# Kernel tuning notes

Measured on AMD Instinct MI355X. Metric: run time of the kernel, lower is better.

The kernel has to match this reference:

```python
import jax, jax.numpy as jnp
import numpy as np

N, E, F_IN, H, EF, G, GFD = 50000, 800000, 64, 128, 8, 10, 2
NEG_SLOPE = 0.2  # PyG GATv2Conv default negative_slope


def _gatv2_layer(x, src, dst, edge_attr, Wl, bl, Wr, br, We, att, bias):
    # PyG GATv2Conv, heads=1, concat=True, share_weights=False
    n = x.shape[0]
    xl = x @ Wl + bl            # source transform [N,H]
    xr = x @ Wr + br            # target transform [N,H]
    e = edge_attr @ We          # edge embedding   [E,H]
    s = jax.nn.leaky_relu(xl[src] + xr[dst] + e, NEG_SLOPE)  # [E,H]
    logits = s @ att            # [E]
    # numerically-stable segment softmax over destination nodes
    mx = jax.ops.segment_max(logits, dst, num_segments=n)
    mx = jnp.where(jnp.isfinite(mx), mx, 0.0)
    ex = jnp.exp(logits - mx[dst])
    den = jax.ops.segment_sum(ex, dst, num_segments=n)
    alpha = ex / jnp.maximum(den[dst], 1e-16)
    out = jax.ops.segment_sum(alpha[:, None] * xl[src], dst, num_segments=n)
    return out + bias


def _forward(x, edge_index, edge_attr, graph_features, num_graphs, params, head_W, head_b):
    src, dst = edge_index[0], edge_index[1]
    for (Wl, bl, Wr, br, We, att, bias) in params:
        x = jax.nn.relu(_gatv2_layer(x, src, dst, edge_attr, Wl, bl, Wr, br, We, att, bias))
        # dropout p=0.0 / eval mode: no-op
    n_nodes = x.shape[0] // num_graphs
    # faithful replication of the torch reshape chain (graph_feature_dim == 2):
    # graph_features.T [GFD,G] -> unsqueeze(2) -> repeat to [GFD,G,Np] -> view(G,GFD,Np)
    # -> cat(unbind(0), dim=1) -> [GFD, G*Np]
    gf = jnp.broadcast_to(graph_features.T[:, :, None], (GFD, num_graphs, n_nodes))
    gf = gf.reshape(num_graphs, GFD, n_nodes)
    gf = gf.transpose(1, 0, 2).reshape(GFD, num_graphs * n_nodes)
    x = jnp.concatenate([x, gf.T], axis=1)  # [N, H+GFD]
    return x @ head_W + head_b


def setup_inputs():
    key = jax.random.key(0)
    ks = list(jax.random.split(key, 32))
    p = lambda k, s: jax.random.normal(k, s, jnp.float32) * 0.05
    inp = {
        'x': jax.random.normal(ks[0], (N, F_IN), jnp.float32),
        'edge_index': jax.random.randint(ks[1], (2, E), 0, N),
        'edge_attr': jax.random.normal(ks[2], (E, EF), jnp.float32),
        'graph_features': jax.random.normal(ks[3], (G, GFD), jnp.float32),
        'num_graphs': G,
    }
    i = 4
    for l in range(3):
        fin = F_IN if l == 0 else H
        inp[f'Wl{l}'] = p(ks[i], (fin, H)); i += 1
        inp[f'bl{l}'] = jnp.zeros((H,), jnp.float32)
        inp[f'Wr{l}'] = p(ks[i], (fin, H)); i += 1
        inp[f'br{l}'] = jnp.zeros((H,), jnp.float32)
        inp[f'We{l}'] = p(ks[i], (EF, H)); i += 1
        inp[f'att{l}'] = p(ks[i], (H,)); i += 1
        inp[f'bias{l}'] = jnp.zeros((H,), jnp.float32)
    inp['head_W'] = p(ks[i], (H + GFD, 1))
    inp['head_b'] = jnp.zeros((1,), jnp.float32)
    return inp


def reference(x, edge_index, edge_attr, graph_features, num_graphs,
              Wl0, bl0, Wr0, br0, We0, att0, bias0,
              Wl1, bl1, Wr1, br1, We1, att1, bias1,
              Wl2, bl2, Wr2, br2, We2, att2, bias2,
              head_W, head_b):
    params = [(Wl0, bl0, Wr0, br0, We0, att0, bias0),
              (Wl1, bl1, Wr1, br1, We1, att1, bias1),
              (Wl2, bl2, Wr2, br2, We2, att2, bias2)]
    return _forward(x, edge_index, edge_attr, graph_features, num_graphs, params, head_W, head_b)
```

## Files before the change

### kernel.cpp

```cpp
#include <hip/hip_runtime.h>
#include <hip/hip_bf16.h>
#include <math.h>

#define NN 50000
#define EE 800000
#define F_IN 64
#define HH 128
#define EF 8
#define GG 10
#define GFD 2
#define NEG_SLOPE 0.2f
#define NB 64

__device__ __forceinline__ void fma4(float4& a, float s, const float4& b) {
  a.x = fmaf(s, b.x, a.x); a.y = fmaf(s, b.y, a.y);
  a.z = fmaf(s, b.z, a.z); a.w = fmaf(s, b.w, a.w);
}
__device__ __forceinline__ float lrelu1(float x) {
  return fmaxf(x, NEG_SLOPE * x);
}

template <int CTRL>
__device__ __forceinline__ float dpp_add(float v) {
  int p = __builtin_amdgcn_update_dpp(0, __float_as_int(v), CTRL, 0xf, 0xf, true);
  return v + __int_as_float(p);
}
__device__ __forceinline__ float red32(float v) {
  v = dpp_add<0xB1>(v);
  v = dpp_add<0x4E>(v);
  v = dpp_add<0x141>(v);
  v = dpp_add<0x140>(v);
  v += __int_as_float(__builtin_amdgcn_ds_swizzle(__float_as_int(v), 0x401F));
  return v;
}

__global__ __launch_bounds__(256) void lin2_kernel(
    const float* __restrict__ x, int fin,
    const float* __restrict__ Wl, const float* __restrict__ bl,
    const float* __restrict__ Wr, const float* __restrict__ br,
    float* __restrict__ xl, float* __restrict__ xr, int n_nodes) {
  __shared__ float xs[64 * 128];
  const int tid = threadIdx.x;
  const int base = blockIdx.x * 64;
  int nrows = n_nodes - base; if (nrows > 64) nrows = 64;

  const int total4 = (nrows * fin) >> 2;
  const float4* xsrc = (const float4*)(x + (size_t)base * fin);
  float4* xd = (float4*)xs;
  for (int i = tid; i < total4; i += 256) xd[i] = xsrc[i];
  __syncthreads();

  const int lane = tid & 63;
  const int w = tid >> 6;
  const int c = lane * 2;

  float accl0[16], accl1[16], accr0[16], accr1[16];
#pragma unroll
  for (int j = 0; j < 16; j++) { accl0[j]=0.f; accl1[j]=0.f; accr0[j]=0.f; accr1[j]=0.f; }

  const float* xrow = xs + (w * 16) * fin;
  for (int k = 0; k < fin; k += 4) {
    float2 wl0 = *(const float2*)(Wl + (size_t)k * HH + c);
    float2 wl1 = *(const float2*)(Wl + (size_t)(k + 1) * HH + c);
    float2 wl2 = *(const float2*)(Wl + (size_t)(k + 2) * HH + c);
    float2 wl3 = *(const float2*)(Wl + (size_t)(k + 3) * HH + c);
    float2 wr0 = *(const float2*)(Wr + (size_t)k * HH + c);
    float2 wr1 = *(const float2*)(Wr + (size_t)(k + 1) * HH + c);
    float2 wr2 = *(const float2*)(Wr + (size_t)(k + 2) * HH + c);
    float2 wr3 = *(const float2*)(Wr + (size_t)(k + 3) * HH + c);
#pragma unroll
    for (int j = 0; j < 16; j++) {
      float4 xv = *(const float4*)(xrow + j * fin + k);
      accl0[j] = fmaf(xv.x, wl0.x, accl0[j]);
      accl1[j] = fmaf(xv.x, wl0.y, accl1[j]);
      accr0[j] = fmaf(xv.x, wr0.x, accr0[j]);
      accr1[j] = fmaf(xv.x, wr0.y, accr1[j]);
      accl0[j] = fmaf(xv.y, wl1.x, accl0[j]);
      accl1[j] = fmaf(xv.y, wl1.y, accl1[j]);
      accr0[j] = fmaf(xv.y, wr1.x, accr0[j]);
      accr1[j] = fmaf(xv.y, wr1.y, accr1[j]);
      accl0[j] = fmaf(xv.z, wl2.x, accl0[j]);
      accl1[j] = fmaf(xv.z, wl2.y, accl1[j]);
      accr0[j] = fmaf(xv.z, wr2.x, accr0[j]);
      accr1[j] = fmaf(xv.z, wr2.y, accr1[j]);
      accl0[j] = fmaf(xv.w, wl3.x, accl0[j]);
      accl1[j] = fmaf(xv.w, wl3.y, accl1[j]);
      accr0[j] = fmaf(xv.w, wr3.x, accr0[j]);
      accr1[j] = fmaf(xv.w, wr3.y, accr1[j]);
    }
  }
  float2 blv = *(const float2*)(bl + c);
  float2 brv = *(const float2*)(br + c);
#pragma unroll
  for (int j = 0; j < 16; j++) {
    int n = base + w * 16 + j;
    if (n < n_nodes) {
      *(float2*)(xl + (size_t)n * HH + c) = make_float2(accl0[j] + blv.x, accl1[j] + blv.y);
      *(float2*)(xr + (size_t)n * HH + c) = make_float2(accr0[j] + brv.x, accr1[j] + brv.y);
    }
  }
}

__global__ __launch_bounds__(256) void hist_kernel(const int* __restrict__ dst,
                                                   int* __restrict__ hist, int ne) {
  int i = blockIdx.x * blockDim.x + threadIdx.x;
  if (i < ne) atomicAdd(&hist[dst[i]], 1);
}

__global__ __launch_bounds__(1024) void reduce_kernel(const int* __restrict__ hist,
                                                      int* __restrict__ bsum, int n) {
  __shared__ int wsum[16];
  const int tid = threadIdx.x;
  const int lane = tid & 63, w = tid >> 6;
  int i = blockIdx.x * 1024 + tid;
  int v = (i < n) ? hist[i] : 0;
#pragma unroll
  for (int off = 32; off; off >>= 1) v += __shfl_xor(v, off);
  if (lane == 0) wsum[w] = v;
  __syncthreads();
  if (tid < 16) {
    int s = wsum[tid];
#pragma unroll
    for (int off = 8; off; off >>= 1) s += __shfl_xor(s, off);
    if (tid == 0) bsum[blockIdx.x] = s;
  }
}

__global__ __launch_bounds__(64) void scanb_kernel(const int* __restrict__ bsum,
                                                   int* __restrict__ bbase,
                                                   int* __restrict__ offs, int nb, int n) {
  const int tid = threadIdx.x;
  int v = (tid < nb) ? bsum[tid] : 0;
  int inc = v;
#pragma unroll
  for (int d = 1; d < 64; d <<= 1) {
    int t2 = __shfl_up(inc, d);
    if (tid >= d) inc += t2;
  }
  if (tid < nb) bbase[tid] = inc - v;
  if (tid == 63) offs[n] = inc;
}

__global__ __launch_bounds__(1024) void scanc_kernel(const int* __restrict__ hist,
                                                     const int* __restrict__ bbase,
                                                     int* __restrict__ offs,
                                                     int* __restrict__ cursor, int n) {
  __shared__ int wsum[16], wpre[16];
  const int tid = threadIdx.x;
  const int lane = tid & 63, w = tid >> 6;
  int i = blockIdx.x * 1024 + tid;
  int orig = (i < n) ? hist[i] : 0;
  int v = orig;
#pragma unroll
  for (int d = 1; d < 64; d <<= 1) {
    int t2 = __shfl_up(v, d);
    if (lane >= d) v += t2;
  }
  if (lane == 63) wsum[w] = v;
  __syncthreads();
  if (tid < 16) {
    int s = wsum[tid];
    int inc = s;
#pragma unroll
    for (int d = 1; d < 16; d <<= 1) {
      int t2 = __shfl_up(inc, d);
      if (tid >= d) inc += t2;
    }
    wpre[tid] = inc - s;
  }
  __syncthreads();
  if (i < n) {
    int ex = bbase[blockIdx.x] + wpre[w] + (v - orig);
    offs[i] = ex; cursor[i] = ex;
  }
}

__global__ __launch_bounds__(256) void scatter_kernel(
    const int* __restrict__ src, const int* __restrict__ dst,
    int* __restrict__ cursor, int* __restrict__ pk,
    const float4* __restrict__ ea4, float4* __restrict__ eas, int ne) {
  int i = blockIdx.x * blockDim.x + threadIdx.x;
  if (i < ne) {
    int d = dst[i];
    int pos = atomicAdd(&cursor[d], 1);
    pk[pos] = src[i] * 512;
    float4 a = ea4[i * 2], b = ea4[i * 2 + 1];
    eas[pos * 2] = a; eas[pos * 2 + 1] = b;
  }
}

__global__ __launch_bounds__(256) void deg_hist_kernel(const int* __restrict__ offs,
                                                       int* __restrict__ hist2, int n) {
  __shared__ int lhist[NB];
  const int tid = threadIdx.x;
  int i = blockIdx.x * 256 + tid;
  if (tid < NB) lhist[tid] = 0;
  __syncthreads();
  if (i < n) {
    int d = offs[i + 1] - offs[i];
    int key = NB - 1 - min(d, NB - 1);
    atomicAdd(&lhist[key], 1);
  }
  __syncthreads();
  if (tid < NB && lhist[tid]) atomicAdd(&hist2[tid], lhist[tid]);
}

__global__ __launch_bounds__(64) void scan64_kernel(const int* __restrict__ hist2,
                                                    int* __restrict__ cursor2) {
  const int tid = threadIdx.x;
  int v = hist2[tid];
  int inc = v;
#pragma unroll
  for (int d = 1; d < 64; d <<= 1) {
    int t2 = __shfl_up(inc, d);
    if (tid >= d) inc += t2;
  }
  cursor2[tid] = inc - v;
}

__global__ __launch_bounds__(256) void deg_scatter_kernel(const int* __restrict__ offs,
                                                          int* __restrict__ cursor2,
                                                          int4* __restrict__ meta4, int n) {
  __shared__ int lhist[NB];
  __shared__ int lbase[NB];
  const int tid = threadIdx.x;
  int i = blockIdx.x * 256 + tid;
  if (tid < NB) lhist[tid] = 0;
  __syncthreads();
  int key = 0, rank = 0, bb = 0, ee = 0;
  const bool valid = (i < n);
  if (valid) {
    bb = offs[i]; ee = offs[i + 1];
    int d = ee - bb;
    key = NB - 1 - min(d, NB - 1);
    rank = atomicAdd(&lhist[key], 1);
  }
  __syncthreads();
  if (tid < NB && lhist[tid]) lbase[tid] = atomicAdd(&cursor2[tid], lhist[tid]);
  __syncthreads();
  if (valid) meta4[lbase[key] + rank] = make_int4(bb, ee, i, 0);
}

__global__ __launch_bounds__(256, 4) void gat_fused_kernel(
    const float* __restrict__ xl, const float* __restrict__ xr,
    const float* __restrict__ eas, const float* __restrict__ We,
    const float* __restrict__ att,
    const int* __restrict__ pk, const int4* __restrict__ meta4,
    const float* __restrict__ bias,
    float* __restrict__ xout, int n_nodes,
    float* __restrict__ out_head, const float* __restrict__ hw,
    const float* __restrict__ hb) {
  const int lane = threadIdx.x & 63;
  const int g = lane >> 5, t = lane & 31;
  const int c = t * 4;
  const int tb = t * 16;
  const int nwaves = gridDim.x * 4;

  float4 we[EF];
#pragma unroll
  for (int k = 0; k < EF; k++) we[k] = *(const float4*)(We + k * HH + c);
  const float4 at = *(const float4*)(att + c);
  const float4 bi = *(const float4*)(bias + c);
  const char* xlb = (const char*)xl;
  const char* easb = (const char*)eas;
  float4 hwv = make_float4(0.f, 0.f, 0.f, 0.f);
  float hw0 = 0.f, hw1 = 0.f, hb0 = 0.f;
  if (out_head) {
    hwv = *(const float4*)(hw + c);
    hw0 = hw[HH]; hw1 = hw[HH + 1]; hb0 = hb[0];
  }

  int wid = blockIdx.x * 4 + (threadIdx.x >> 6);
  if (wid >= n_nodes) return;
  int4 mt = meta4[wid];
  float4 vr = *(const float4*)(xr + (size_t)mt.z * HH + c);

  while (true) {
    const int b = mt.x, e = mt.y, node = mt.z;
    const int deg = e - b;
    const int nwid = wid + nwaves;
    const bool hasN = nwid < n_nodes;
    int4 mtN = mt;
    if (hasN) mtN = meta4[nwid];

    float4 o;
    if (deg == 0) {
      o.x = fmaxf(bi.x, 0.f); o.y = fmaxf(bi.y, 0.f);
      o.z = fmaxf(bi.z, 0.f); o.w = fmaxf(bi.w, 0.f);
    } else {
      const int emax = e - 1;
      float4 acc = make_float4(0.f, 0.f, 0.f, 0.f);
      float den = 0.f;
      float4 vlA, eaPA, eaQA, vlB, eaPB, eaQB;

#define LOADS(VL, EP, EQ, IDX)                                      \
  do {                                                              \
    int _cx = min((IDX), emax);                                     \
    EP = *(const float4*)(easb + (_cx << 5));                       \
    EQ = *(const float4*)(easb + (_cx << 5) + 16);                  \
    int _ob = pk[_cx];                                              \
    VL = *(const float4*)(xlb + (_ob + tb));                        \
  } while (0)

#define PROCESS(VL, EP, EQ, IDX)                                     \
  do {                                                               \
    float4 s = make_float4(VL.x + vr.x, VL.y + vr.y, VL.z + vr.z,    \
                           VL.w + vr.w);                             \
    fma4(s, EP.x, we[0]); fma4(s, EP.y, we[1]);                      \
    fma4(s, EP.z, we[2]); fma4(s, EP.w, we[3]);                      \
    fma4(s, EQ.x, we[4]); fma4(s, EQ.y, we[5]);                      \
    fma4(s, EQ.z, we[6]); fma4(s, EQ.w, we[7]);                      \
    float v = lrelu1(s.x) * at.x;                                    \
    v = fmaf(lrelu1(s.y), at.y, v);                                  \
    v = fmaf(lrelu1(s.z), at.z, v);                                  \
    v = fmaf(lrelu1(s.w), at.w, v);                                  \
    v = red32(v);                                                    \
    const float p = ((IDX) < e) ? __expf(v) : 0.f;                   \
    den += p;                                                        \
    fma4(acc, p, VL);                                                \
  } while (0)

      int idx = b + g;
      LOADS(vlA, eaPA, eaQA, idx);
      LOADS(vlB, eaPB, eaQB, idx + 2);

      const int nit = (deg + 3) >> 2;
      for (int j = 0; j < nit; j++) {
        PROCESS(vlA, eaPA, eaQA, idx);
        LOADS(vlA, eaPA, eaQA, idx + 4);
        PROCESS(vlB, eaPB, eaQB, idx + 2);
        LOADS(vlB, eaPB, eaQB, idx + 6);
        idx += 4;
      }
#undef LOADS
#undef PROCESS

      den += __shfl_xor(den, 32);
      acc.x += __shfl_xor(acc.x, 32);
      acc.y += __shfl_xor(acc.y, 32);
      acc.z += __shfl_xor(acc.z, 32);
      acc.w += __shfl_xor(acc.w, 32);

      const float inv = 1.f / fmaxf(den, 1e-16f);
      o.x = fmaxf(fmaf(acc.x, inv, bi.x), 0.f);
      o.y = fmaxf(fmaf(acc.y, inv, bi.y), 0.f);
      o.z = fmaxf(fmaf(acc.z, inv, bi.z), 0.f);
      o.w = fmaxf(fmaf(acc.w, inv, bi.w), 0.f);
    }

    float4 vrN = vr;
    if (hasN) vrN = *(const float4*)(xr + (size_t)mtN.z * HH + c);

    if (!out_head) {
      if (g == 0) *(float4*)(xout + (size_t)node * HH + c) = o;
    } else {
      float hv = o.x * hwv.x + o.y * hwv.y + o.z * hwv.z + o.w * hwv.w;
      hv = red32(hv);
      if (lane == 0) {
        int k = node / (NN / GG);
        int i0 = 2 * k, i1 = 2 * k + 1;
        float gf0 = xout[(i0 % GG) * GFD + (i0 / GG)];
        float gf1 = xout[(i1 % GG) * GFD + (i1 / GG)];
        out_head[node] = hv + gf0 * hw0 + gf1 * hw1 + hb0;
      }
    }

    if (!hasN) break;
    wid = nwid; mt = mtN; vr = vrN;
  }
}

extern "C" void kernel_launch(void* const* d_in, const int* in_sizes, int n_in,
                              void* d_out, int out_size, void* d_ws, size_t ws_size,
                              hipStream_t stream) {
  const float* x_in = (const float*)d_in[0];
  const int*   eidx = (const int*)d_in[1];
  const float* ea   = (const float*)d_in[2];
  const float* gf   = (const float*)d_in[3];
  const int* src = eidx;
  const int* dst = eidx + EE;
  const float* head_W = (const float*)d_in[26];
  const float* head_b = (const float*)d_in[27];
  float* out = (float*)d_out;

  const int NCHUNK = (NN + 1023) / 1024;

  float* P      = (float*)d_ws;
  float* Q      = P + (size_t)NN * HH;
  float* R      = Q + (size_t)NN * HH;
  float* eas    = R + (size_t)NN * HH;
  int*   pk     = (int*)(eas + (size_t)EE * EF);
  int*   hist   = pk + EE;
  int*   offs   = hist + NN;
  int*   cursor = offs + NN + 1;
  int*   hist2  = cursor + NN;
  int*   cursor2= hist2 + NB;
  int*   bsum   = cursor2 + NB;
  int*   bbase  = bsum + NCHUNK;
  int4*  meta4  = (int4*)(((size_t)(bbase + NCHUNK) + 15) & ~(size_t)15);

  (void)hipMemsetAsync(hist, 0, NN * sizeof(int), stream);
  (void)hipMemsetAsync(hist2, 0, NB * sizeof(int), stream);
  hist_kernel<<<(EE + 255) / 256, 256, 0, stream>>>(dst, hist, EE);
  reduce_kernel<<<NCHUNK, 1024, 0, stream>>>(hist, bsum, NN);
  scanb_kernel<<<1, 64, 0, stream>>>(bsum, bbase, offs, NCHUNK, NN);
  scanc_kernel<<<NCHUNK, 1024, 0, stream>>>(hist, bbase, offs, cursor, NN);
  scatter_kernel<<<(EE + 255) / 256, 256, 0, stream>>>(src, dst, cursor, pk,
                                                       (const float4*)ea, (float4*)eas, EE);
  deg_hist_kernel<<<(NN + 255) / 256, 256, 0, stream>>>(offs, hist2, NN);
  scan64_kernel<<<1, 64, 0, stream>>>(hist2, cursor2);
  deg_scatter_kernel<<<(NN + 255) / 256, 256, 0, stream>>>(offs, cursor2, meta4, NN);

  const float* xcur = x_in;
  int fin = F_IN;
  for (int l = 0; l < 3; l++) {
    const float* Wl   = (const float*)d_in[5 + 7 * l + 0];
    const float* bl   = (const float*)d_in[5 + 7 * l + 1];
    const float* Wr   = (const float*)d_in[5 + 7 * l + 2];
    const float* br   = (const float*)d_in[5 + 7 * l + 3];
    const float* We   = (const float*)d_in[5 + 7 * l + 4];
    const float* att  = (const float*)d_in[5 + 7 * l + 5];
    const float* bias = (const float*)d_in[5 + 7 * l + 6];

    lin2_kernel<<<(NN + 63) / 64, 256, 0, stream>>>(xcur, fin, Wl, bl, Wr, br, P, Q, NN);
    if (l < 2) {
      gat_fused_kernel<<<2048, 256, 0, stream>>>(P, Q, eas, We, att, pk, meta4,
                                                 bias, R, NN, nullptr, nullptr, nullptr);
    } else {
      gat_fused_kernel<<<2048, 256, 0, stream>>>(P, Q, eas, We, att, pk, meta4,
                                                 bias, (float*)gf, NN, out, head_W, head_b);
    }
    xcur = R;
    fin = HH;
  }
}
```

Before: 494.5 us.

## Fuse independent preprocessing kernels and use packed v2f math in GAT edge loop

Merges the layer-0 linear transform with the destination histogram into one launch, and the edge scatter with the degree histogram into another, selecting the role by block index. This cuts kernel launches and lets independent work share the GPU. The two histogram buffers become adjacent so a single memset clears both. The GAT edge loop is rewritten with 2-wide float vectors and elementwise FMA so the compiler can emit packed FP32 instructions, at the cost of more register shuffling and possible pressure under the 4-blocks launch bound.

```diff
diff --git a/kernel.cpp b/kernel.cpp
--- a/kernel.cpp
+++ b/kernel.cpp
@@ -12,10 +12,12 @@
 #define NEG_SLOPE 0.2f
 #define NB 64
 
-__device__ __forceinline__ void fma4(float4& a, float s, const float4& b) {
-  a.x = fmaf(s, b.x, a.x); a.y = fmaf(s, b.y, a.y);
-  a.z = fmaf(s, b.z, a.z); a.w = fmaf(s, b.w, a.w);
-}
+typedef float v2f __attribute__((ext_vector_type(2)));
+__device__ __forceinline__ v2f fma2(v2f a, v2f b, v2f c) {
+  return __builtin_elementwise_fma(a, b, c);
+}
+__device__ __forceinline__ v2f bc2(float x) { v2f r; r.x = x; r.y = x; return r; }
+
 __device__ __forceinline__ float lrelu1(float x) {
   return fmaxf(x, NEG_SLOPE * x);
 }
@@ -34,14 +36,14 @@
   return v;
 }
 
-__global__ __launch_bounds__(256) void lin2_kernel(
-    const float* __restrict__ x, int fin,
+__device__ __forceinline__ void lin2_body(
+    int bid, const float* __restrict__ x, int fin,
     const float* __restrict__ Wl, const float* __restrict__ bl,
     const float* __restrict__ Wr, const float* __restrict__ br,
     float* __restrict__ xl, float* __restrict__ xr, int n_nodes) {
   __shared__ float xs[64 * 128];
   const int tid = threadIdx.x;
-  const int base = blockIdx.x * 64;
+  const int base = bid * 64;
   int nrows = n_nodes - base; if (nrows > 64) nrows = 64;
 
   const int total4 = (nrows * fin) >> 2;
@@ -101,10 +103,30 @@
   }
 }
 
-__global__ __launch_bounds__(256) void hist_kernel(const int* __restrict__ dst,
-                                                   int* __restrict__ hist, int ne) {
-  int i = blockIdx.x * blockDim.x + threadIdx.x;
+__global__ __launch_bounds__(256) void lin2_kernel(
+    const float* __restrict__ x, int fin,
+    const float* __restrict__ Wl, const float* __restrict__ bl,
+    const float* __restrict__ Wr, const float* __restrict__ br,
+    float* __restrict__ xl, float* __restrict__ xr, int n_nodes) {
+  lin2_body(blockIdx.x, x, fin, Wl, bl, Wr, br, xl, xr, n_nodes);
+}
+
+__device__ __forceinline__ void hist_body(int bid, const int* __restrict__ dst,
+                                          int* __restrict__ hist, int ne) {
+  int i = bid * 256 + threadIdx.x;
   if (i < ne) atomicAdd(&hist[dst[i]], 1);
+}
+
+__global__ __launch_bounds__(256) void fusedA_kernel(
+    int nl2, const float* __restrict__ x, int fin,
+    const float* __restrict__ Wl, const float* __restrict__ bl,
+    const float* __restrict__ Wr, const float* __restrict__ br,
+    float* __restrict__ xl, float* __restrict__ xr, int n_nodes,
+    const int* __restrict__ dst, int* __restrict__ hist, int ne) {
+  if ((int)blockIdx.x < nl2)
+    lin2_body(blockIdx.x, x, fin, Wl, bl, Wr, br, xl, xr, n_nodes);
+  else
+    hist_body(blockIdx.x - nl2, dst, hist, ne);
 }
 
 __global__ __launch_bounds__(1024) void reduce_kernel(const int* __restrict__ hist,
@@ -175,11 +197,11 @@
   }
 }
 
-__global__ __launch_bounds__(256) void scatter_kernel(
-    const int* __restrict__ src, const int* __restrict__ dst,
+__device__ __forceinline__ void scatter_body(
+    int bid, const int* __restrict__ src, const int* __restrict__ dst,
     int* __restrict__ cursor, int* __restrict__ pk,
     const float4* __restrict__ ea4, float4* __restrict__ eas, int ne) {
-  int i = blockIdx.x * blockDim.x + threadIdx.x;
+  int i = bid * 256 + threadIdx.x;
   if (i < ne) {
     int d = dst[i];
     int pos = atomicAdd(&cursor[d], 1);
@@ -189,11 +211,11 @@
   }
 }
 
-__global__ __launch_bounds__(256) void deg_hist_kernel(const int* __restrict__ offs,
-                                                       int* __restrict__ hist2, int n) {
+__device__ __forceinline__ void deg_hist_body(int bid, const int* __restrict__ offs,
+                                              int* __restrict__ hist2, int n) {
   __shared__ int lhist[NB];
   const int tid = threadIdx.x;
-  int i = blockIdx.x * 256 + tid;
+  int i = bid * 256 + tid;
   if (tid < NB) lhist[tid] = 0;
   __syncthreads();
   if (i < n) {
@@ -203,6 +225,17 @@
   }
   __syncthreads();
   if (tid < NB && lhist[tid]) atomicAdd(&hist2[tid], lhist[tid]);
+}
+
+__global__ __launch_bounds__(256) void fusedB_kernel(
+    int nsc, const int* __restrict__ src, const int* __restrict__ dst,
+    int* __restrict__ cursor, int* __restrict__ pk,
+    const float4* __restrict__ ea4, float4* __restrict__ eas, int ne,
+    const int* __restrict__ offs, int* __restrict__ hist2, int n) {
+  if ((int)blockIdx.x < nsc)
+    scatter_body(blockIdx.x, src, dst, cursor, pk, ea4, eas, ne);
+  else
+    deg_hist_body(blockIdx.x - nsc, offs, hist2, n);
 }
 
 __global__ __launch_bounds__(64) void scan64_kernel(const int* __restrict__ hist2,
@@ -256,9 +289,13 @@
   const int tb = t * 16;
   const int nwaves = gridDim.x * 4;
 
-  float4 we[EF];
-#pragma unroll
-  for (int k = 0; k < EF; k++) we[k] = *(const float4*)(We + k * HH + c);
+  v2f wea[EF], web[EF];
+#pragma unroll
+  for (int k = 0; k < EF; k++) {
+    float4 w4 = *(const float4*)(We + k * HH + c);
+    wea[k].x = w4.x; wea[k].y = w4.y;
+    web[k].x = w4.z; web[k].y = w4.w;
+  }
   const float4 at = *(const float4*)(att + c);
   const float4 bi = *(const float4*)(bias + c);
   const char* xlb = (const char*)xl;
@@ -273,7 +310,7 @@
   int wid = blockIdx.x * 4 + (threadIdx.x >> 6);
   if (wid >= n_nodes) return;
   int4 mt = meta4[wid];
-  float4 vr = *(const float4*)(xr + (size_t)mt.z * HH + c);
+  float4 vr4 = *(const float4*)(xr + (size_t)mt.z * HH + c);
 
   while (true) {
     const int b = mt.x, e = mt.y, node = mt.z;
@@ -283,72 +320,88 @@
     int4 mtN = mt;
     if (hasN) mtN = meta4[nwid];
 
+    v2f vra; vra.x = vr4.x; vra.y = vr4.y;
+    v2f vrb; vrb.x = vr4.z; vrb.y = vr4.w;
+
     float4 o;
     if (deg == 0) {
       o.x = fmaxf(bi.x, 0.f); o.y = fmaxf(bi.y, 0.f);
       o.z = fmaxf(bi.z, 0.f); o.w = fmaxf(bi.w, 0.f);
     } else {
       const int emax = e - 1;
-      float4 acc = make_float4(0.f, 0.f, 0.f, 0.f);
+      v2f acc0 = bc2(0.f), acc1 = bc2(0.f);
       float den = 0.f;
-      float4 vlA, eaPA, eaQA, vlB, eaPB, eaQB;
-
-#define LOADS(VL, EP, EQ, IDX)                                      \
+      v2f vlAa, vlAb, epA0, epA1, eqA0, eqA1;
+      v2f vlBa, vlBb, epB0, epB1, eqB0, eqB1;
+
+#define LOADS(VLa, VLb, P0, P1, Q0, Q1, IDX)                        \
   do {                                                              \
     int _cx = min((IDX), emax);                                     \
-    EP = *(const float4*)(easb + (_cx << 5));                       \
-    EQ = *(const float4*)(easb + (_cx << 5) + 16);                  \
+    float4 _ep = *(const float4*)(easb + (_cx << 5));               \
+    float4 _eq = *(const float4*)(easb + (_cx << 5) + 16);          \
     int _ob = pk[_cx];                                              \
-    VL = *(const float4*)(xlb + (_ob + tb));                        \
+    float4 _vl = *(const float4*)(xlb + (_ob + tb));                \
+    P0.x = _ep.x; P0.y = _ep.y; P1.x = _ep.z; P1.y = _ep.w;         \
+    Q0.x = _eq.x; Q0.y = _eq.y; Q1.x = _eq.z; Q1.y = _eq.w;         \
+    VLa.x = _vl.x; VLa.y = _vl.y; VLb.x = _vl.z; VLb.y = _vl.w;     \
   } while (0)
 
-#define PROCESS(VL, EP, EQ, IDX)                                     \
+#define PROCESS(VLa, VLb, P0, P1, Q0, Q1, IDX)                       \
   do {                                                               \
-    float4 s = make_float4(VL.x + vr.x, VL.y + vr.y, VL.z + vr.z,    \
-                           VL.w + vr.w);                             \
-    fma4(s, EP.x, we[0]); fma4(s, EP.y, we[1]);                      \
-    fma4(s, EP.z, we[2]); fma4(s, EP.w, we[3]);                      \
-    fma4(s, EQ.x, we[4]); fma4(s, EQ.y, we[5]);                      \
-    fma4(s, EQ.z, we[6]); fma4(s, EQ.w, we[7]);                      \
-    float v = lrelu1(s.x) * at.x;                                    \
-    v = fmaf(lrelu1(s.y), at.y, v);                                  \
-    v = fmaf(lrelu1(s.z), at.z, v);                                  \
-    v = fmaf(lrelu1(s.w), at.w, v);                                  \
+    v2f s0 = VLa + vra;                                              \
+    v2f s1 = VLb + vrb;                                              \
+    s0 = fma2(bc2(P0.x), wea[0], s0); s1 = fma2(bc2(P0.x), web[0], s1); \
+    s0 = fma2(bc2(P0.y), wea[1], s0); s1 = fma2(bc2(P0.y), web[1], s1); \
+    s0 = fma2(bc2(P1.x), wea[2], s0); s1 = fma2(bc2(P1.x), web[2], s1); \
+    s0 = fma2(bc2(P1.y), wea[3], s0); s1 = fma2(bc2(P1.y), web[3], s1); \
+    s0 = fma2(bc2(Q0.x), wea[4], s0); s1 = fma2(bc2(Q0.x), web[4], s1); \
+    s0 = fma2(bc2(Q0.y), wea[5], s0); s1 = fma2(bc2(Q0.y), web[5], s1); \
+    s0 = fma2(bc2(Q1.x), wea[6], s0); s1 = fma2(bc2(Q1.x), web[6], s1); \
+    s0 = fma2(bc2(Q1.y), wea[7], s0); s1 = fma2(bc2(Q1.y), web[7], s1); \
+    v2f m0 = s0 * bc2(NEG_SLOPE);                                    \
+    v2f m1 = s1 * bc2(NEG_SLOPE);                                    \
+    float l0 = fmaxf(s0.x, m0.x), l1 = fmaxf(s0.y, m0.y);            \
+    float l2 = fmaxf(s1.x, m1.x), l3 = fmaxf(s1.y, m1.y);            \
+    float v = l0 * at.x;                                             \
+    v = fmaf(l1, at.y, v);                                           \
+    v = fmaf(l2, at.z, v);                                           \
+    v = fmaf(l3, at.w, v);                                           \
     v = red32(v);                                                    \
     const float p = ((IDX) < e) ? __expf(v) : 0.f;                   \
     den += p;                                                        \
-    fma4(acc, p, VL);                                                \
+    acc0 = fma2(bc2(p), VLa, acc0);                                  \
+    acc1 = fma2(bc2(p), VLb, acc1);                                  \
   } while (0)
 
       int idx = b + g;
-      LOADS(vlA, eaPA, eaQA, idx);
-      LOADS(vlB, eaPB, eaQB, idx + 2);
+      LOADS(vlAa, vlAb, epA0, epA1, eqA0, eqA1, idx);
+      LOADS(vlBa, vlBb, epB0, epB1, eqB0, eqB1, idx + 2);
 
       const int nit = (deg + 3) >> 2;
       for (int j = 0; j < nit; j++) {
-        PROCESS(vlA, eaPA, eaQA, idx);
-        LOADS(vlA, eaPA, eaQA, idx + 4);
-        PROCESS(vlB, eaPB, eaQB, idx + 2);
-        LOADS(vlB, eaPB, eaQB, idx + 6);
+        PROCESS(vlAa, vlAb, epA0, epA1, eqA0, eqA1, idx);
+        LOADS(vlAa, vlAb, epA0, epA1, eqA0, eqA1, idx + 4);
+        PROCESS(vlBa, vlBb, epB0, epB1, eqB0, eqB1, idx + 2);
+        LOADS(vlBa, vlBb, epB0, epB1, eqB0, eqB1, idx + 6);
         idx += 4;
       }
 #undef LOADS
 #undef PROCESS
 
       den += __shfl_xor(den, 32);
-      acc.x += __shfl_xor(acc.x, 32);
-      acc.y += __shfl_xor(acc.y, 32);
-      acc.z += __shfl_xor(acc.z, 32);
-      acc.w += __shfl_xor(acc.w, 32);
+      float a0 = acc0.x + __shfl_xor(acc0.x, 32);
+      float a1 = acc0.y + __shfl_xor(acc0.y, 32);
+      float a2 = acc1.x + __shfl_xor(acc1.x, 32);
+      float a3 = acc1.y + __shfl_xor(acc1.y, 32);
 
       const float inv = 1.f / fmaxf(den, 1e-16f);
-      o.x = fmaxf(fmaf(acc.x, inv, bi.x), 0.f);
-      o.y = fmaxf(fmaf(acc.y, inv, bi.y), 0.f);
-      o.z = fmaxf(fmaf(acc.z, inv, bi.z), 0.f);
-      o.w = fmaxf(fmaf(acc.w, inv, bi.w), 0.f);
-    }
-
-    float4 vrN = vr;
+      o.x = fmaxf(fmaf(a0, inv, bi.x), 0.f);
+      o.y = fmaxf(fmaf(a1, inv, bi.y), 0.f);
+      o.z = fmaxf(fmaf(a2, inv, bi.z), 0.f);
+      o.w = fmaxf(fmaf(a3, inv, bi.w), 0.f);
+    }
+
+    float4 vrN = vr4;
     if (hasN) vrN = *(const float4*)(xr + (size_t)mtN.z * HH + c);
 
     if (!out_head) {
@@ -366,7 +419,7 @@
     }
 
     if (!hasN) break;
-    wid = nwid; mt = mtN; vr = vrN;
+    wid = nwid; mt = mtN; vr4 = vrN;
   }
 }
 
@@ -384,6 +437,9 @@
   float* out = (float*)d_out;
 
   const int NCHUNK = (NN + 1023) / 1024;
+  const int NL2B = (NN + 63) / 64;
+  const int NHB  = (EE + 255) / 256;
+  const int NDB  = (NN + 255) / 256;
 
   float* P      = (float*)d_ws;
   float* Q      = P + (size_t)NN * HH;
@@ -391,38 +447,41 @@
   float* eas    = R + (size_t)NN * HH;
   int*   pk     = (int*)(eas + (size_t)EE * EF);
   int*   hist   = pk + EE;
-  int*   offs   = hist + NN;
+  int*   hist2  = hist + NN;
+  int*   offs   = hist2 + NB;
   int*   cursor = offs + NN + 1;
-  int*   hist2  = cursor + NN;
-  int*   cursor2= hist2 + NB;
+  int*   cursor2= cursor + NN;
   int*   bsum   = cursor2 + NB;
   int*   bbase  = bsum + NCHUNK;
   int4*  meta4  = (int4*)(((size_t)(bbase + NCHUNK) + 15) & ~(size_t)15);
 
-  (void)hipMemsetAsync(hist, 0, NN * sizeof(int), stream);
-  (void)hipMemsetAsync(hist2, 0, NB * sizeof(int), stream);
-  hist_kernel<<<(EE + 255) / 256, 256, 0, stream>>>(dst, hist, EE);
+  const float* Wl0 = (const float*)d_in[5], *bl0 = (const float*)d_in[6];
+  const float* Wr0 = (const float*)d_in[7], *br0 = (const float*)d_in[8];
+
+  (void)hipMemsetAsync(hist, 0, (NN + NB) * sizeof(int), stream);
+  fusedA_kernel<<<NL2B + NHB, 256, 0, stream>>>(NL2B, x_in, F_IN, Wl0, bl0, Wr0, br0,
+                                                P, Q, NN, dst, hist, EE);
   reduce_kernel<<<NCHUNK, 1024, 0, stream>>>(hist, bsum, NN);
   scanb_kernel<<<1, 64, 0, stream>>>(bsum, bbase, offs, NCHUNK, NN);
   scanc_kernel<<<NCHUNK, 1024, 0, stream>>>(hist, bbase, offs, cursor, NN);
-  scatter_kernel<<<(EE + 255) / 256, 256, 0, stream>>>(src, dst, cursor, pk,
-                                                       (const float4*)ea, (float4*)eas, EE);
-  deg_hist_kernel<<<(NN + 255) / 256, 256, 0, stream>>>(offs, hist2, NN);
+  fusedB_kernel<<<NHB + NDB, 256, 0, stream>>>(NHB, src, dst, cursor, pk,
+                                               (const float4*)ea, (float4*)eas, EE,
+                                               offs, hist2, NN);
   scan64_kernel<<<1, 64, 0, stream>>>(hist2, cursor2);
-  deg_scatter_kernel<<<(NN + 255) / 256, 256, 0, stream>>>(offs, cursor2, meta4, NN);
-
-  const float* xcur = x_in;
-  int fin = F_IN;
+  deg_scatter_kernel<<<NDB, 256, 0, stream>>>(offs, cursor2, meta4, NN);
+
   for (int l = 0; l < 3; l++) {
-    const float* Wl   = (const float*)d_in[5 + 7 * l + 0];
-    const float* bl   = (const float*)d_in[5 + 7 * l + 1];
-    const float* Wr   = (const float*)d_in[5 + 7 * l + 2];
-    const float* br   = (const float*)d_in[5 + 7 * l + 3];
     const float* We   = (const float*)d_in[5 + 7 * l + 4];
     const float* att  = (const float*)d_in[5 + 7 * l + 5];
     const float* bias = (const float*)d_in[5 + 7 * l + 6];
 
-    lin2_kernel<<<(NN + 63) / 64, 256, 0, stream>>>(xcur, fin, Wl, bl, Wr, br, P, Q, NN);
+    if (l > 0) {
+      const float* Wl = (const float*)d_in[5 + 7 * l + 0];
+      const float* bl = (const float*)d_in[5 + 7 * l + 1];
+      const float* Wr = (const float*)d_in[5 + 7 * l + 2];
+      const float* br = (const float*)d_in[5 + 7 * l + 3];
+      lin2_kernel<<<NL2B, 256, 0, stream>>>(R, HH, Wl, bl, Wr, br, P, Q, NN);
+    }
     if (l < 2) {
       gat_fused_kernel<<<2048, 256, 0, stream>>>(P, Q, eas, We, att, pk, meta4,
                                                  bias, R, NN, nullptr, nullptr, nullptr);
@@ -430,7 +489,5 @@
       gat_fused_kernel<<<2048, 256, 0, stream>>>(P, Q, eas, We, att, pk, meta4,
                                                  bias, (float*)gf, NN, out, head_W, head_b);
     }
-    xcur = R;
-    fin = HH;
-  }
-}
+  }
+}
```

After: 482.7 us. 1.02x faster.
